# Optimization experiments

Measured on AMD Instinct MI355X. Metric: run time of the kernel, lower is better.

Reference implementation:

```python
import jax, jax.numpy as jnp
import numpy as np

B, V, E, H, L = 1024, 8192, 64, 64, 16
TAU = 1.2
SOS_ID, EOS_ID = 1, 2


def setup_inputs() -> dict:
    key = jax.random.key(0)
    ks = jax.random.split(key, 7)
    hidden_state = jax.random.normal(ks[0], (B, H), dtype=jnp.float32)
    # embedding ~ N(0, 0.1) as in reset_parameters
    embedding = 0.1 * jax.random.normal(ks[1], (V, E), dtype=jnp.float32)
    # LSTMCell weight_ih: xavier uniform, weight_hh: orthogonal
    bound = float(np.sqrt(6.0 / (4 * H + E)))
    W_ih = jax.random.uniform(ks[2], (4 * H, E), minval=-bound, maxval=bound, dtype=jnp.float32)
    a = jax.random.normal(ks[3], (4 * H, H), dtype=jnp.float32)
    q, r = jnp.linalg.qr(a)
    W_hh = q * jnp.sign(jnp.diagonal(r))  # [4H, H] orthogonal columns
    b_ih = jnp.zeros((4 * H,), jnp.float32)
    b_hh = jnp.zeros((4 * H,), jnp.float32).at[H:2 * H].set(1.0)  # forget-gate bias = 1
    # linear_out is zero-init in the torch code; use small random values so the
    # math under test is non-trivial (init is data, not math).
    W_out = 0.02 * jax.random.normal(ks[4], (V, H), dtype=jnp.float32)
    b_out = jnp.zeros((V,), jnp.float32)
    # Precomputed standard Gumbel noise for deterministic sampling
    u = jax.random.uniform(ks[5], (L, B, V), minval=1e-10, maxval=1.0, dtype=jnp.float32)
    gumbels = -jnp.log(-jnp.log(u))
    return {
        'hidden_state': hidden_state, 'embedding': embedding,
        'W_ih': W_ih, 'W_hh': W_hh, 'b_ih': b_ih, 'b_hh': b_hh,
        'W_out': W_out, 'b_out': b_out, 'gumbels': gumbels,
    }


def reference(hidden_state, embedding, W_ih, W_hh, b_ih, b_hh, W_out, b_out, gumbels):
    b, h_dim = hidden_state.shape
    v = embedding.shape[0]
    n_steps = gumbels.shape[0]
    initial_length = n_steps + 1

    sos_onehot = jnp.zeros((b, v), hidden_state.dtype).at[:, SOS_ID].set(1.0)

    def step(carry, xs):
        h, c, prev_token, seq_lengths, ent = carry
        g, i = xs
        emb = prev_token @ embedding                                   # [b, E]
        gates = emb @ W_ih.T + b_ih + h @ W_hh.T + b_hh                # [b, 4H]
        ii, ff, gg, oo = jnp.split(gates, 4, axis=-1)                  # torch order i,f,g,o
        c = jax.nn.sigmoid(ff) * c + jax.nn.sigmoid(ii) * jnp.tanh(gg)
        h = jax.nn.sigmoid(oo) * jnp.tanh(c)
        logits = h @ W_out.T + b_out                                   # [b, V]
        logp = jax.nn.log_softmax(logits, axis=-1)
        p = jnp.exp(logp)
        ent = ent - jnp.sum(p * logp, axis=-1)
        # RelaxedOneHotCategorical rsample: softmax((log p + gumbel) / tau)
        y = jax.nn.softmax((logp + g) / TAU, axis=-1)
        y_hard = jax.nn.one_hot(jnp.argmax(y, axis=-1), v, dtype=y.dtype)
        token = jax.lax.stop_gradient(y_hard - y) + y                  # straight-through
        max_pred = jnp.max(token, axis=-1)
        vocab_idx = jnp.argmax(token, axis=-1)
        mask = (vocab_idx == EOS_ID) & (max_pred == 1.0) & (seq_lengths == initial_length)
        seq_lengths = jnp.where(mask, i + 2, seq_lengths)              # seq_pos + 1 with seq_pos = i+1
        return (h, c, token, seq_lengths, ent), (token, emb)

    c0 = jnp.zeros_like(hidden_state)
    seq0 = jnp.full((b,), initial_length, jnp.int32)
    ent0 = jnp.zeros((b,), hidden_state.dtype)
    (_, _, _, seq_lengths, ent), (tokens, embeds) = jax.lax.scan(
        step, (hidden_state, c0, sos_onehot, seq0, ent0),
        (gumbels, jnp.arange(n_steps, dtype=jnp.int32)))

    output = jnp.concatenate([sos_onehot[:, None, :], jnp.swapaxes(tokens, 0, 1)], axis=1)  # [b, L+1, V]
    embeds = jnp.swapaxes(embeds, 0, 1)                                                      # [b, L, E]
    entropy = jnp.mean(ent) / n_steps
    return output, seq_lengths, entropy, hidden_state, embeds
```

## Files before the change

### kernel.cpp

```cpp
#include <hip/hip_runtime.h>
#include <cmath>

#define B_ 1024
#define V_ 8192
#define E_ 64
#define H_ 64
#define L_ 16
#define SOS 1
#define EOS 2

#define ONEHOT_OFF 0ull
#define SEQ_OFF    142606336ull
#define ENT_OFF    142607360ull
#define HID_OFF    142607361ull
#define EMB_OFF    142672897ull

__global__ __launch_bounds__(256, 2) void logits_stats_kernel(
    const float* __restrict__ Wout, const float* __restrict__ bout,
    const float* __restrict__ gstep,
    const float* __restrict__ h,
    float* __restrict__ pm, float* __restrict__ pS, float* __restrict__ pT,
    float* __restrict__ pbv, int* __restrict__ pbi)
{
    __shared__ float wV[256][68];
    __shared__ float hV[16][68];

    const int t  = threadIdx.x;
    const int rg = blockIdx.x >> 3;
    const int vs = blockIdx.x & 7;
    const int rowBase = rg * 16;
    const int tv = t & 63;
    const int tr = t >> 6;
    const int r0 = tr * 4;

    {
        const int rl = t >> 4;
        const int k0 = (t & 15) * 4;
        float4 hv = *(const float4*)(h + (size_t)(rowBase + rl) * 64 + k0);
        *(float4*)&hV[rl][k0] = hv;
    }

    float m[4], S[4], T[4], bv[4];
    int   bi[4];
#pragma unroll
    for (int r = 0; r < 4; ++r) {
        m[r] = -INFINITY; S[r] = 0.f; T[r] = 0.f; bv[r] = -INFINITY; bi[r] = 0;
    }

    for (int cc = 0; cc < 4; ++cc) {
        const int vglob = vs * 1024 + cc * 256;
        __syncthreads();
#pragma unroll
        for (int j = 0; j < 16; ++j) {
            const int f  = (t + 256 * j) * 4;
            const int vl = f >> 6;
            const int k0 = f & 63;
            float4 w = *(const float4*)(Wout + (size_t)(vglob + vl) * 64 + k0);
            *(float4*)&wV[vl][k0] = w;
        }
        __syncthreads();

        float acc[4][4];
#pragma unroll
        for (int r = 0; r < 4; ++r)
#pragma unroll
            for (int j = 0; j < 4; ++j) acc[r][j] = 0.f;

#pragma unroll 4
        for (int k4 = 0; k4 < 16; ++k4) {
            float4 wv[4], hv[4];
#pragma unroll
            for (int j = 0; j < 4; ++j) wv[j] = *(const float4*)&wV[tv + 64 * j][k4 * 4];
#pragma unroll
            for (int r = 0; r < 4; ++r) hv[r] = *(const float4*)&hV[r0 + r][k4 * 4];
#pragma unroll
            for (int r = 0; r < 4; ++r)
#pragma unroll
                for (int j = 0; j < 4; ++j)
                    acc[r][j] += hv[r].x * wv[j].x + hv[r].y * wv[j].y +
                                 hv[r].z * wv[j].z + hv[r].w * wv[j].w;
        }

#pragma unroll
        for (int j = 0; j < 4; ++j) {
            const int v  = vglob + 64 * j + tv;
            const float bo = bout[v];
#pragma unroll
            for (int r = 0; r < 4; ++r) {
                const int row = rowBase + r0 + r;
                const float l = acc[r][j] + bo;
                const float s = l + gstep[(size_t)row * V_ + v];
                if (s > bv[r]) { bv[r] = s; bi[r] = v; }
                const float mn = fmaxf(m[r], l);
                const float e  = __expf(-fabsf(l - m[r]));
                const bool nw  = l > m[r];
                const float a  = nw ? e : 1.f;
                const float b2 = nw ? 1.f : e;
                S[r] = S[r] * a + b2;
                T[r] = T[r] * a + l * b2;
                m[r] = mn;
            }
        }
    }

#pragma unroll
    for (int off = 1; off < 64; off <<= 1) {
#pragma unroll
        for (int r = 0; r < 4; ++r) {
            const float mo  = __shfl_xor(m[r], off);
            const float So  = __shfl_xor(S[r], off);
            const float To  = __shfl_xor(T[r], off);
            const float bvo = __shfl_xor(bv[r], off);
            const int   bio = __shfl_xor(bi[r], off);
            const float mn = fmaxf(m[r], mo);
            const float ea = __expf(m[r] - mn);
            const float eb = __expf(mo - mn);
            S[r] = S[r] * ea + So * eb;
            T[r] = T[r] * ea + To * eb;
            m[r] = mn;
            if (bvo > bv[r] || (bvo == bv[r] && bio < bi[r])) { bv[r] = bvo; bi[r] = bio; }
        }
    }
    if (tv == 0) {
#pragma unroll
        for (int r = 0; r < 4; ++r) {
            const int row = rowBase + r0 + r;
            const int o = vs * 1024 + row;
            pm[o] = m[r]; pS[o] = S[r]; pT[o] = T[r]; pbv[o] = bv[r]; pbi[o] = bi[r];
        }
    }
}

__global__ __launch_bounds__(256) void combine_lstm_kernel(
    const float* __restrict__ emb_table,
    const float* __restrict__ W_ih, const float* __restrict__ W_hh,
    const float* __restrict__ b_ih, const float* __restrict__ b_hh,
    const float* __restrict__ hidden_in,
    float* __restrict__ h, float* __restrict__ c,
    float* __restrict__ ent, int* __restrict__ seq,
    const float* __restrict__ pm, const float* __restrict__ pS,
    const float* __restrict__ pT, const float* __restrict__ pbv,
    const int* __restrict__ pbi,
    float* __restrict__ out, int step)
{
    __shared__ float wrow[256][132];
    __shared__ float xcat[8][128];
    __shared__ float gatesL[8][256];
    __shared__ int   toksL[8];
    __shared__ float entL[8];

    const int t = threadIdx.x;
    const int rowBase = blockIdx.x * 8;

    if (step >= 0) {
        if (t < 8) {
            const int row = rowBase + t;
            float m = -INFINITY, S = 0.f, T = 0.f, bv = -INFINITY; int bi = 0;
            for (int s = 0; s < 8; ++s) {
                const int o = s * 1024 + row;
                const float ms = pm[o], Ss = pS[o], Ts = pT[o], bvs = pbv[o];
                const int bis = pbi[o];
                const float mn = fmaxf(m, ms);
                const float ea = __expf(m - mn), eb = __expf(ms - mn);
                S = S * ea + Ss * eb; T = T * ea + Ts * eb; m = mn;
                if (bvs > bv || (bvs == bv && bis < bi)) { bv = bvs; bi = bis; }
            }
            const float lse  = m + logf(S);
            const float entc = lse - T / S;
            const int tok = bi;
            out[ONEHOT_OFF + (size_t)row * (17 * 8192) + (size_t)(step + 1) * 8192 + tok] = 1.0f;
            const float ev = (step == 0) ? entc : (ent[row] + entc);
            ent[row] = ev;
            int sl = (step == 0) ? (L_ + 1) : seq[row];
            if (tok == EOS && sl == (L_ + 1)) sl = step + 2;
            seq[row] = sl;
            toksL[t] = tok;
            entL[t] = ev;
            if (step == 15) out[SEQ_OFF + row] = (float)sl;
        }
    } else {
        if (t < 8) {
            const int row = rowBase + t;
            toksL[t] = SOS;
            out[ONEHOT_OFF + (size_t)row * (17 * 8192) + SOS] = 1.0f;
        }
    }
    __syncthreads();

    if (step == 15) {
        if (t == 0) {
            float a = 0.f;
            for (int r = 0; r < 8; ++r) a += entL[r];
            atomicAdd(out + ENT_OFF, a * (1.0f / (1024.0f * 16.0f)));
        }
        return;
    }

#pragma unroll
    for (int j = 0; j < 16; ++j) {
        const int f  = (t + 256 * j) * 4;
        const int gr = f >> 6;
        const int k0 = f & 63;
        *(float4*)&wrow[gr][k0]      = *(const float4*)(W_ih + f);
        *(float4*)&wrow[gr][64 + k0] = *(const float4*)(W_hh + f);
    }
    if (t < 128) {
        const int r = t >> 4, k0 = (t & 15) * 4;
        const int row = rowBase + r;
        const int tk = (step < 0) ? SOS : toksL[r];
        float4 evv = *(const float4*)(emb_table + (size_t)tk * 64 + k0);
        *(float4*)&xcat[r][k0] = evv;
        const size_t eo = EMB_OFF + ((size_t)row * 16 + (size_t)(step + 1)) * 64 + k0;
        out[eo + 0] = evv.x; out[eo + 1] = evv.y; out[eo + 2] = evv.z; out[eo + 3] = evv.w;
    } else {
        const int tt = t - 128;
        const int r = tt >> 4, k0 = (tt & 15) * 4;
        const int row = rowBase + r;
        const float* hsrc = (step < 0) ? (hidden_in + (size_t)row * 64 + k0)
                                       : (h + (size_t)row * 64 + k0);
        float4 hv = *(const float4*)hsrc;
        *(float4*)&xcat[r][64 + k0] = hv;
    }
    __syncthreads();

    {
        const float bia = b_ih[t] + b_hh[t];
        float acc[8];
#pragma unroll
        for (int r = 0; r < 8; ++r) acc[r] = bia;
        for (int k4 = 0; k4 < 32; ++k4) {
            const float4 w4 = *(const float4*)&wrow[t][k4 * 4];
#pragma unroll
            for (int r = 0; r < 8; ++r) {
                const float4 x4 = *(const float4*)&xcat[r][k4 * 4];
                acc[r] += x4.x * w4.x + x4.y * w4.y + x4.z * w4.z + x4.w * w4.w;
            }
        }
#pragma unroll
        for (int r = 0; r < 8; ++r) gatesL[r][t] = acc[r];
    }
    __syncthreads();

#pragma unroll
    for (int q = 0; q < 2; ++q) {
        const int u = t + q * 256;
        const int r = u >> 6, uu = u & 63;
        const int row = rowBase + r;
        const float ii = gatesL[r][uu];
        const float ff = gatesL[r][64 + uu];
        const float gg = gatesL[r][128 + uu];
        const float oo = gatesL[r][192 + uu];
        const float cp = (step < 0) ? 0.f : c[(size_t)row * 64 + uu];
        const float si = 1.f / (1.f + expf(-ii));
        const float sf = 1.f / (1.f + expf(-ff));
        const float so = 1.f / (1.f + expf(-oo));
        const float cn = sf * cp + si * tanhf(gg);
        const float hn = so * tanhf(cn);
        c[(size_t)row * 64 + uu] = cn;
        h[(size_t)row * 64 + uu] = hn;
    }
}

extern "C" void kernel_launch(void* const* d_in, const int* in_sizes, int n_in,
                              void* d_out, int out_size, void* d_ws, size_t ws_size,
                              hipStream_t stream) {
    (void)in_sizes; (void)ws_size;
    if (n_in < 9) return;
    const float* hidden    = (const float*)d_in[0];
    const float* embedding = (const float*)d_in[1];
    const float* W_ih      = (const float*)d_in[2];
    const float* W_hh      = (const float*)d_in[3];
    const float* b_ih      = (const float*)d_in[4];
    const float* b_hh      = (const float*)d_in[5];
    const float* W_out     = (const float*)d_in[6];
    const float* b_out     = (const float*)d_in[7];
    const float* gumbels   = (const float*)d_in[8];
    float* out = (float*)d_out;

    float* wsf = (float*)d_ws;
    float* h   = wsf;
    float* c   = wsf + 65536;
    float* ent = wsf + 131072;
    int*   seq = (int*)(wsf + 132096);
    float* pm  = wsf + 133120;
    float* pS  = pm + 8192;
    float* pT  = pS + 8192;
    float* pbv = pT + 8192;
    int*   pbi = (int*)(pbv + 8192);

    hipMemsetAsync(d_out, 0, (size_t)out_size * sizeof(float), stream);
    hipMemcpyAsync(out + HID_OFF, hidden, (size_t)B_ * H_ * sizeof(float),
                   hipMemcpyDeviceToDevice, stream);

    combine_lstm_kernel<<<128, 256, 0, stream>>>(embedding, W_ih, W_hh, b_ih, b_hh,
        hidden, h, c, ent, seq, pm, pS, pT, pbv, pbi, out, -1);
    for (int i = 0; i < 16; ++i) {
        logits_stats_kernel<<<512, 256, 0, stream>>>(W_out, b_out,
            gumbels + (size_t)i * B_ * V_, h, pm, pS, pT, pbv, pbi);
        combine_lstm_kernel<<<128, 256, 0, stream>>>(embedding, W_ih, W_hh, b_ih, b_hh,
            hidden, h, c, ent, seq, pm, pS, pT, pbv, pbi, out, i);
    }
}
```

Measured before the change: 1.554 ms.

## Fold one-hot output zeroing into per-step logits kernels instead of a bulk memset

Replaces the full-output hipMemsetAsync (about 570MB) with distributed zeroing. A small init kernel zeroes the SOS slab and sets the SOS one-hot. Each logits_stats launch zeroes its own step's 8192-wide slab for its 16 rows using nontemporal stores. This overlaps the zero-fill traffic with the compute-bound logits work and avoids a separate pass. The combine kernel then writes the 1.0 entries. It relies on the step-ordered kernels to keep zero writes before the one-hot writes, and it assumes the other output regions (hidden, embeds, seq) are fully written elsewhere.

```diff
diff --git a/kernel.cpp b/kernel.cpp
--- a/kernel.cpp
+++ b/kernel.cpp
@@ -9,18 +9,35 @@
 #define SOS 1
 #define EOS 2
 
+typedef float f32x4 __attribute__((ext_vector_type(4)));
+
 #define ONEHOT_OFF 0ull
 #define SEQ_OFF    142606336ull
 #define ENT_OFF    142607360ull
 #define HID_OFF    142607361ull
 #define EMB_OFF    142672897ull
 
+__global__ __launch_bounds__(256) void init_zero_kernel(float* __restrict__ out)
+{
+    const int t = threadIdx.x;
+    const int row = blockIdx.x;
+    float* slab = out + ONEHOT_OFF + (size_t)row * (17 * 8192);
+#pragma unroll
+    for (int j = 0; j < 8; ++j) {
+        f32x4 z = {0.f, 0.f, 0.f, 0.f};
+        if (j == 0 && t == 0) z.y = 1.0f;
+        __builtin_nontemporal_store(z, (f32x4*)(slab + j * 1024 + t * 4));
+    }
+    if (row == 0 && t == 1) out[ENT_OFF] = 0.f;
+}
+
 __global__ __launch_bounds__(256, 2) void logits_stats_kernel(
     const float* __restrict__ Wout, const float* __restrict__ bout,
     const float* __restrict__ gstep,
     const float* __restrict__ h,
     float* __restrict__ pm, float* __restrict__ pS, float* __restrict__ pT,
-    float* __restrict__ pbv, int* __restrict__ pbi)
+    float* __restrict__ pbv, int* __restrict__ pbi,
+    float* __restrict__ out, int step)
 {
     __shared__ float wV[256][68];
     __shared__ float hV[16][68];
@@ -38,6 +55,16 @@
         const int k0 = (t & 15) * 4;
         float4 hv = *(const float4*)(h + (size_t)(rowBase + rl) * 64 + k0);
         *(float4*)&hV[rl][k0] = hv;
+    }
+
+    {
+        const f32x4 z = {0.f, 0.f, 0.f, 0.f};
+        const size_t slab = ONEHOT_OFF + (size_t)(step + 1) * 8192 + (size_t)(vs * 1024 + t * 4);
+#pragma unroll
+        for (int r = 0; r < 16; ++r) {
+            __builtin_nontemporal_store(z,
+                (f32x4*)(out + (size_t)(rowBase + r) * (17 * 8192) + slab));
+        }
     }
 
     float m[4], S[4], T[4], bv[4];
@@ -179,11 +206,7 @@
             if (step == 15) out[SEQ_OFF + row] = (float)sl;
         }
     } else {
-        if (t < 8) {
-            const int row = rowBase + t;
-            toksL[t] = SOS;
-            out[ONEHOT_OFF + (size_t)row * (17 * 8192) + SOS] = 1.0f;
-        }
+        if (t < 8) toksL[t] = SOS;
     }
     __syncthreads();
 
@@ -264,7 +287,7 @@
 extern "C" void kernel_launch(void* const* d_in, const int* in_sizes, int n_in,
                               void* d_out, int out_size, void* d_ws, size_t ws_size,
                               hipStream_t stream) {
-    (void)in_sizes; (void)ws_size;
+    (void)in_sizes; (void)ws_size; (void)out_size;
     if (n_in < 9) return;
     const float* hidden    = (const float*)d_in[0];
     const float* embedding = (const float*)d_in[1];
@@ -288,15 +311,15 @@
     float* pbv = pT + 8192;
     int*   pbi = (int*)(pbv + 8192);
 
-    hipMemsetAsync(d_out, 0, (size_t)out_size * sizeof(float), stream);
-    hipMemcpyAsync(out + HID_OFF, hidden, (size_t)B_ * H_ * sizeof(float),
-                   hipMemcpyDeviceToDevice, stream);
+    (void)hipMemcpyAsync(out + HID_OFF, hidden, (size_t)B_ * H_ * sizeof(float),
+                         hipMemcpyDeviceToDevice, stream);
+    init_zero_kernel<<<1024, 256, 0, stream>>>(out);
 
     combine_lstm_kernel<<<128, 256, 0, stream>>>(embedding, W_ih, W_hh, b_ih, b_hh,
         hidden, h, c, ent, seq, pm, pS, pT, pbv, pbi, out, -1);
     for (int i = 0; i < 16; ++i) {
         logits_stats_kernel<<<512, 256, 0, stream>>>(W_out, b_out,
-            gumbels + (size_t)i * B_ * V_, h, pm, pS, pT, pbv, pbi);
+            gumbels + (size_t)i * B_ * V_, h, pm, pS, pT, pbv, pbi, out, i);
         combine_lstm_kernel<<<128, 256, 0, stream>>>(embedding, W_ih, W_hh, b_ih, b_hh,
             hidden, h, c, ent, seq, pm, pS, pT, pbv, pbi, out, i);
     }
```

Result: no change. 1.530 ms (-1.5%).
